# Performance work log

Measured on AMD Instinct MI355X. Metric: run time of the kernel, lower is better.

The kernel has to match this reference:

```python
import jax, jax.numpy as jnp
import numpy as np

N = 50000      # nodes
T = 24         # sequence length
D_IN = 16      # lstm input dim
H = 64         # lstm hidden dim
SD = 9         # static feature dim
G_IN, G_HID, G_OUT = 64, 64, 1
E = 1600000    # edges
NUM_GRAPHS = 500


def setup_inputs() -> dict:
    key = jax.random.key(0)
    ks = jax.random.split(key, 16)
    s = 0.1
    return {
        "x": jax.random.normal(ks[0], (N, T, D_IN), dtype=jnp.float32),
        "sdi": jax.random.normal(ks[1], (N, SD), dtype=jnp.float32),
        "edge_index": jax.random.randint(ks[2], (2, E), 0, N, dtype=jnp.int64),
        "batch": jnp.sort(jax.random.randint(ks[3], (N,), 0, NUM_GRAPHS, dtype=jnp.int64)),
        # LSTM params (torch gate order: i, f, g, o)
        "W_ih": s * jax.random.normal(ks[4], (4 * H, D_IN), dtype=jnp.float32),
        "W_hh": s * jax.random.normal(ks[5], (4 * H, H), dtype=jnp.float32),
        "b_ih": s * jax.random.normal(ks[6], (4 * H,), dtype=jnp.float32),
        "b_hh": s * jax.random.normal(ks[7], (4 * H,), dtype=jnp.float32),
        # Linear l1: (hidden + static) -> graph_input
        "l1_W": s * jax.random.normal(ks[8], (G_IN, H + SD), dtype=jnp.float32),
        "l1_b": s * jax.random.normal(ks[9], (G_IN,), dtype=jnp.float32),
        # GCNConv layers (weight stored [out, in] like torch Linear)
        "gcn1_W": s * jax.random.normal(ks[10], (G_HID, G_IN), dtype=jnp.float32),
        "gcn1_b": s * jax.random.normal(ks[11], (G_HID,), dtype=jnp.float32),
        "gcn2_W": s * jax.random.normal(ks[12], (G_OUT, G_HID), dtype=jnp.float32),
        "gcn2_b": s * jax.random.normal(ks[13], (G_OUT,), dtype=jnp.float32),
    }


def _lstm_last_hidden(x, W_ih, W_hh, b_ih, b_hh):
    # x: [N, T, D]; returns final hidden state h_T: [N, H]
    xg = jnp.einsum("ntd,gd->tng", x, W_ih) + (b_ih + b_hh)  # [T, N, 4H]
    h0 = jnp.zeros((x.shape[0], H), x.dtype)
    c0 = jnp.zeros((x.shape[0], H), x.dtype)

    def step(carry, g_t):
        h, c = carry
        g = g_t + h @ W_hh.T
        i, f, gg, o = jnp.split(g, 4, axis=-1)
        i = jax.nn.sigmoid(i)
        f = jax.nn.sigmoid(f)
        gg = jnp.tanh(gg)
        o = jax.nn.sigmoid(o)
        c = f * c + i * gg
        h = o * jnp.tanh(c)
        return (h, c), None

    (h, _), _ = jax.lax.scan(step, (h0, c0), xg)
    return h


def _gcn_conv(x, edge_index, W, b):
    # PyG GCNConv: add self-loops, symmetric normalization, scatter-add at dst.
    n = x.shape[0]
    loop = jnp.arange(n, dtype=edge_index.dtype)
    row = jnp.concatenate([edge_index[0], loop])  # src
    col = jnp.concatenate([edge_index[1], loop])  # dst
    deg = jax.ops.segment_sum(jnp.ones_like(col, dtype=x.dtype), col, num_segments=n)
    dis = jnp.where(deg > 0, jax.lax.rsqrt(jnp.maximum(deg, 1.0)), 0.0)
    norm = dis[row] * dis[col]                    # [E + N]
    h = x @ W.T                                   # [N, out]
    msg = h[row] * norm[:, None]                  # gather + scale
    out = jax.ops.segment_sum(msg, col, num_segments=n)
    return out + b


def reference(x, sdi, edge_index, batch, W_ih, W_hh, b_ih, b_hh,
              l1_W, l1_b, gcn1_W, gcn1_b, gcn2_W, gcn2_b):
    h = _lstm_last_hidden(x, W_ih, W_hh, b_ih, b_hh)       # [N, H]
    z = jnp.concatenate([h, sdi], axis=-1) @ l1_W.T + l1_b  # [N, G_IN]
    z = jax.nn.relu(_gcn_conv(z, edge_index, gcn1_W, gcn1_b))
    z = _gcn_conv(z, edge_index, gcn2_W, gcn2_b)            # [N, 1]
    # global mean pool over graph ids
    sums = jax.ops.segment_sum(z, batch, num_segments=NUM_GRAPHS)
    cnts = jax.ops.segment_sum(jnp.ones((z.shape[0],), z.dtype), batch, num_segments=NUM_GRAPHS)
    pooled = sums / jnp.maximum(cnts, 1.0)[:, None]         # [G, 1]
    return pooled.reshape(-1)
```

## Files before the change

### kernel.cpp

```cpp
#include <hip/hip_runtime.h>
#include <hip/hip_bf16.h>

#define N_NODES 50000
#define T_SEQ 24
#define D_IN 16
#define H_DIM 64
#define SD 9
#define E_EDGES 1600000
#define NUM_GRAPHS 500
#define NBLK 196

typedef _Float16 half8 __attribute__((ext_vector_type(8)));
typedef _Float16 half4 __attribute__((ext_vector_type(4)));
typedef float floatx4 __attribute__((ext_vector_type(4)));

__device__ __forceinline__ float fsig(float x) {
    return __fdividef(1.0f, 1.0f + __expf(-x));
}
__device__ __forceinline__ float ftanh(float x) {
    return 1.0f - __fdividef(2.0f, 1.0f + __expf(2.0f * x));
}

__global__ __launch_bounds__(256, 2) void lstm_mfma(
    const float* __restrict__ x,
    const float* __restrict__ W_ih, const float* __restrict__ W_hh,
    const float* __restrict__ b_ih, const float* __restrict__ b_hh,
    const float* __restrict__ Wc, const float* __restrict__ bc,
    const float* __restrict__ sdi, const float* __restrict__ dis,
    float* __restrict__ m_out)
{
    __shared__ _Float16 smem[2048 + 24 * 16 * 16];
    _Float16* hb0 = smem;
    _Float16* hb1 = smem + 1024;
    _Float16* xbuf = smem + 2048;

    const int tid  = threadIdx.x;
    const int lane = tid & 63;
    const int w    = tid >> 6;
    const int lr   = lane & 15;
    const int lg   = lane >> 4;
    const int nbase = blockIdx.x * 16;

    half8 bw[4][3];
    float bias[4];
#pragma unroll
    for (int ct = 0; ct < 4; ct++) {
        const int r = ct * 64 + w * 16 + lr;
        bias[ct] = b_ih[r] + b_hh[r];
#pragma unroll
        for (int kt = 0; kt < 2; kt++) {
            const float* p = W_hh + r * 64 + kt * 32 + 8 * lg;
            half8 f;
#pragma unroll
            for (int e = 0; e < 8; e++) f[e] = (_Float16)p[e];
            bw[ct][kt] = f;
        }
        half8 f = {(_Float16)0, (_Float16)0, (_Float16)0, (_Float16)0,
                   (_Float16)0, (_Float16)0, (_Float16)0, (_Float16)0};
        if (lg < 2) {
            const float* p = W_ih + r * 16 + 8 * lg;
#pragma unroll
            for (int e = 0; e < 8; e++) f[e] = (_Float16)p[e];
        }
        bw[ct][2] = f;
    }

    half8 bwc[3];
    {
        const int fr = w * 16 + lr;
#pragma unroll
        for (int kt = 0; kt < 2; kt++) {
            const float* p = Wc + fr * 73 + kt * 32 + 8 * lg;
            half8 f;
#pragma unroll
            for (int e = 0; e < 8; e++) f[e] = (_Float16)p[e];
            bwc[kt] = f;
        }
        half8 f = {(_Float16)0, (_Float16)0, (_Float16)0, (_Float16)0,
                   (_Float16)0, (_Float16)0, (_Float16)0, (_Float16)0};
#pragma unroll
        for (int e = 0; e < 8; e++) {
            const int k2 = 8 * lg + e;
            if (k2 < 9) f[e] = (_Float16)Wc[fr * 73 + 64 + k2];
            else if (k2 == 9) f[e] = (_Float16)bc[fr];
        }
        bwc[2] = f;
    }

#pragma unroll
    for (int it = 0; it < 6; it++) {
        const int f4 = tid + it * 256;
        const int fi = f4 * 4;
        const int n  = fi / 384;
        const int rem = fi - n * 384;
        const int t  = rem >> 4;
        const int d  = rem & 15;
        const float4 v = *reinterpret_cast<const float4*>(
            x + (size_t)(nbase + n) * 384 + rem);
        half4 hv = {(_Float16)v.x, (_Float16)v.y, (_Float16)v.z, (_Float16)v.w};
        *reinterpret_cast<half4*>(&xbuf[t * 256 + n * 16 + d]) = hv;
    }
    if (tid < 128) { ((int*)hb0)[tid] = 0; ((int*)hb0)[tid + 128] = 0; ((int*)hb0)[tid + 256] = 0; ((int*)hb0)[tid + 384] = 0; }

    const int u = w * 16 + lr;
    int ra[2];
#pragma unroll
    for (int kt = 0; kt < 2; kt++)
        ra[kt] = lr * 64 + 8 * ((4 * kt + lg) ^ (lr & 7));
    int woff[4];
#pragma unroll
    for (int j = 0; j < 4; j++) {
        const int nj = 4 * lg + j;
        woff[j] = nj * 64 + (u & 7) + 8 * ((u >> 3) ^ (nj & 7));
    }
    const int xro = lr * 16 + 8 * (lg & 1);

    float c_reg[4];
#pragma unroll
    for (int j = 0; j < 4; j++) c_reg[j] = 0.0f;

    __syncthreads();

    auto step = [&](int tl, _Float16* hR, _Float16* hW) {
        floatx4 acc[4];
#pragma unroll
        for (int ct = 0; ct < 4; ct++) {
            floatx4 a = {bias[ct], bias[ct], bias[ct], bias[ct]};
            acc[ct] = a;
        }
        const half8 ax = *reinterpret_cast<const half8*>(&xbuf[tl * 256 + xro]);
        const half8 ah0 = *reinterpret_cast<const half8*>(&hR[ra[0]]);
        const half8 ah1 = *reinterpret_cast<const half8*>(&hR[ra[1]]);
#pragma unroll
        for (int ct = 0; ct < 4; ct++)
            acc[ct] = __builtin_amdgcn_mfma_f32_16x16x32_f16(ah0, bw[ct][0], acc[ct], 0, 0, 0);
#pragma unroll
        for (int ct = 0; ct < 4; ct++)
            acc[ct] = __builtin_amdgcn_mfma_f32_16x16x32_f16(ah1, bw[ct][1], acc[ct], 0, 0, 0);
#pragma unroll
        for (int ct = 0; ct < 4; ct++)
            acc[ct] = __builtin_amdgcn_mfma_f32_16x16x32_f16(ax, bw[ct][2], acc[ct], 0, 0, 0);

#pragma unroll
        for (int j = 0; j < 4; j++) {
            const float ig = fsig(acc[0][j]);
            const float fg = fsig(acc[1][j]);
            const float gg = ftanh(acc[2][j]);
            const float og = fsig(acc[3][j]);
            const float cv = fg * c_reg[j] + ig * gg;
            c_reg[j] = cv;
            const float hv = og * ftanh(cv);
            hW[woff[j]] = (_Float16)hv;
        }
        __syncthreads();
    };

    for (int tb = 0; tb < 6; tb++) {
        const int t0 = tb * 4;
        step(t0 + 0, hb0, hb1);
        step(t0 + 1, hb1, hb0);
        step(t0 + 2, hb0, hb1);
        step(t0 + 3, hb1, hb0);
    }

    half8 axs = {(_Float16)0, (_Float16)0, (_Float16)0, (_Float16)0,
                 (_Float16)0, (_Float16)0, (_Float16)0, (_Float16)0};
#pragma unroll
    for (int e = 0; e < 8; e++) {
        const int k2 = 8 * lg + e;
        if (k2 < 9) axs[e] = (_Float16)sdi[(size_t)(nbase + lr) * SD + k2];
        else if (k2 == 9) axs[e] = (_Float16)1.0f;
    }
    const half8 fh0 = *reinterpret_cast<const half8*>(&hb0[ra[0]]);
    const half8 fh1 = *reinterpret_cast<const half8*>(&hb0[ra[1]]);
    floatx4 am = {0.0f, 0.0f, 0.0f, 0.0f};
    am = __builtin_amdgcn_mfma_f32_16x16x32_f16(fh0, bwc[0], am, 0, 0, 0);
    am = __builtin_amdgcn_mfma_f32_16x16x32_f16(fh1, bwc[1], am, 0, 0, 0);
    am = __builtin_amdgcn_mfma_f32_16x16x32_f16(axs, bwc[2], am, 0, 0, 0);
#pragma unroll
    for (int j = 0; j < 4; j++) {
        const int gn = nbase + 4 * lg + j;
        m_out[(size_t)gn * 64 + u] = am[j] * dis[gn];
    }
}

__global__ void count_deg(const int* __restrict__ ei, int* __restrict__ cnt) {
    int e = blockIdx.x * 256 + threadIdx.x;
    if (e < E_EDGES) {
        int c = ei[E_EDGES + e];
        if ((unsigned)c < N_NODES) atomicAdd(&cnt[c], 1);
    }
}

__global__ __launch_bounds__(256) void scanA(const int* __restrict__ cnt,
                                             int* __restrict__ ptr,
                                             float* __restrict__ dis,
                                             int* __restrict__ bsum)
{
    __shared__ int wsum[4];
    const int tid = threadIdx.x, lane = tid & 63, wv = tid >> 6;
    const int i = blockIdx.x * 256 + tid;
    const int orig = (i < N_NODES) ? cnt[i] : 0;
    int v = orig;
#pragma unroll
    for (int d = 1; d < 64; d <<= 1) {
        int nb = __shfl_up(v, d, 64);
        if (lane >= d) v += nb;
    }
    if (lane == 63) wsum[wv] = v;
    __syncthreads();
    int woff = 0;
#pragma unroll
    for (int k = 0; k < 3; k++) if (k < wv) woff += wsum[k];
    if (i < N_NODES) {
        ptr[i] = woff + v - orig;
        dis[i] = rsqrtf((float)(orig + 1));
    }
    if (tid == 255) bsum[blockIdx.x] = woff + v;
}

__global__ __launch_bounds__(256) void scanB(const int* __restrict__ bsum,
                                             int* __restrict__ boff,
                                             int* __restrict__ ptr)
{
    __shared__ int wsum[4];
    const int tid = threadIdx.x, lane = tid & 63, wv = tid >> 6;
    const int orig = (tid < NBLK) ? bsum[tid] : 0;
    int v = orig;
#pragma unroll
    for (int d = 1; d < 64; d <<= 1) {
        int nb = __shfl_up(v, d, 64);
        if (lane >= d) v += nb;
    }
    if (lane == 63) wsum[wv] = v;
    __syncthreads();
    int woff = 0;
#pragma unroll
    for (int k = 0; k < 3; k++) if (k < wv) woff += wsum[k];
    if (tid < NBLK) boff[tid] = woff + v - orig;
    if (tid == 255) ptr[N_NODES] = woff + v;
}

__global__ __launch_bounds__(256) void scanC(int* __restrict__ ptr,
                                             const int* __restrict__ boff,
                                             int* __restrict__ cursor)
{
    const int i = blockIdx.x * 256 + threadIdx.x;
    if (i < N_NODES) {
        const int p = ptr[i] + boff[blockIdx.x];
        ptr[i] = p;
        cursor[i] = p;
    }
}

__global__ void fill_csr(const int* __restrict__ ei, int* __restrict__ cursor,
                         int* __restrict__ csr)
{
    int e = blockIdx.x * 256 + threadIdx.x;
    if (e < E_EDGES) {
        int r = ei[e];
        int c = ei[E_EDGES + e];
        if ((unsigned)r < N_NODES && (unsigned)c < N_NODES) {
            int slot = atomicAdd(&cursor[c], 1);
            csr[slot] = r;
        }
    }
}

__global__ void combine_w(const float* __restrict__ g1W, const float* __restrict__ l1W,
                          const float* __restrict__ l1b,
                          float* __restrict__ Wc, float* __restrict__ bc)
{
    int idx = blockIdx.x * 256 + threadIdx.x;
    int o = idx / 74, j = idx - o * 74;
    if (o >= 64) return;
    float acc = 0.0f;
    if (j < 73) {
#pragma unroll 8
        for (int k = 0; k < 64; k++) acc += g1W[o * 64 + k] * l1W[k * 73 + j];
        Wc[o * 73 + j] = acc;
    } else {
#pragma unroll 8
        for (int k = 0; k < 64; k++) acc += g1W[o * 64 + k] * l1b[k];
        bc[o] = acc;
    }
}

__global__ __launch_bounds__(256) void gatherfin1s2(
    const int* __restrict__ ptr, const int* __restrict__ csr,
    const float* __restrict__ m, const float* __restrict__ dis,
    const float* __restrict__ b1, const float* __restrict__ W2,
    float* __restrict__ s2)
{
    const int wid = (blockIdx.x * 256 + threadIdx.x) >> 6;
    const int f = threadIdx.x & 63;
    if (wid >= N_NODES) return;
    const int b = ptr[wid];
    const int e = ptr[wid + 1];
    float a0 = 0.0f, a1 = 0.0f, a2 = 0.0f, a3 = 0.0f;
    int i = b;
    for (; i + 4 <= e; i += 4) {
        const int s0 = csr[i], s1 = csr[i + 1], sc2 = csr[i + 2], s3 = csr[i + 3];
        a0 += m[(size_t)s0 * 64 + f];
        a1 += m[(size_t)s1 * 64 + f];
        a2 += m[(size_t)sc2 * 64 + f];
        a3 += m[(size_t)s3 * 64 + f];
    }
    for (; i < e; i++) a0 += m[(size_t)csr[i] * 64 + f];
    const float self = m[(size_t)wid * 64 + f];
    const float dn = dis[wid];
    const float v = dn * (((a0 + a1) + (a2 + a3)) + self) + b1[f];
    const float z1 = v > 0.0f ? v : 0.0f;
    float p = z1 * W2[f];
#pragma unroll
    for (int off = 32; off >= 1; off >>= 1) p += __shfl_xor(p, off, 64);
    if (f == 0) s2[wid] = dn * p;
}

__global__ void gather2fin(const int* __restrict__ ptr, const int* __restrict__ csr,
                           const float* __restrict__ s2, const float* __restrict__ dis,
                           const float* __restrict__ b2, const int* __restrict__ batch,
                           float* __restrict__ gsum, float* __restrict__ gcnt)
{
    int n = blockIdx.x * 256 + threadIdx.x;
    if (n >= N_NODES) return;
    const int b = ptr[n];
    const int e = ptr[n + 1];
    float a0 = 0.0f, a1 = 0.0f, a2 = 0.0f, a3 = 0.0f;
    int i = b;
    for (; i + 4 <= e; i += 4) {
        a0 += s2[csr[i]];
        a1 += s2[csr[i + 1]];
        a2 += s2[csr[i + 2]];
        a3 += s2[csr[i + 3]];
    }
    for (; i < e; i++) a0 += s2[csr[i]];
    const float z2 = dis[n] * (((a0 + a1) + (a2 + a3)) + s2[n]) + b2[0];
    const int g = batch[n];
    if ((unsigned)g < NUM_GRAPHS) {
        atomicAdd(&gsum[g], z2);
        atomicAdd(&gcnt[g], 1.0f);
    }
}

__global__ void pooldiv(const float* __restrict__ gsum, const float* __restrict__ gcnt,
                        float* __restrict__ out)
{
    int g = blockIdx.x * 256 + threadIdx.x;
    if (g < NUM_GRAPHS) out[g] = gsum[g] / fmaxf(gcnt[g], 1.0f);
}

extern "C" void kernel_launch(void* const* d_in, const int* in_sizes, int n_in,
                              void* d_out, int out_size, void* d_ws, size_t ws_size,
                              hipStream_t stream)
{
    const float* x     = (const float*)d_in[0];
    const float* sdi   = (const float*)d_in[1];
    const int*   ei    = (const int*)d_in[2];
    const int*   batch = (const int*)d_in[3];
    const float* W_ih  = (const float*)d_in[4];
    const float* W_hh  = (const float*)d_in[5];
    const float* b_ih  = (const float*)d_in[6];
    const float* b_hh  = (const float*)d_in[7];
    const float* l1_W  = (const float*)d_in[8];
    const float* l1_b  = (const float*)d_in[9];
    const float* g1_W  = (const float*)d_in[10];
    const float* g1_b  = (const float*)d_in[11];
    const float* g2_W  = (const float*)d_in[12];
    const float* g2_b  = (const float*)d_in[13];
    float* out = (float*)d_out;

    float* ws   = (float*)d_ws;
    float* C    = ws + 6400000;
    float* dis  = ws + 9600000;
    float* s2   = dis + 50000;
    float* gsum = s2 + 50000;
    float* gcnt = gsum + 500;
    int* cnt    = (int*)(gcnt + 500);
    int* ptr    = cnt + 50000;
    int* cursor = ptr + 50001;
    int* csr    = cursor + 50000;
    float* Wc   = (float*)(csr + E_EDGES);
    float* bc   = Wc + 64 * 73;
    int* bsum   = (int*)(bc + 64);
    int* boff   = bsum + NBLK;

    const int featBlocks = (N_NODES * 64 + 255) / 256;
    const int edgeBlocks = (E_EDGES + 255) / 256;

    hipMemsetAsync(cnt, 0, 50000 * sizeof(int), stream);
    hipMemsetAsync(gsum, 0, 1000 * sizeof(float), stream);
    count_deg<<<edgeBlocks, 256, 0, stream>>>(ei, cnt);
    scanA<<<NBLK, 256, 0, stream>>>(cnt, ptr, dis, bsum);
    scanB<<<1, 256, 0, stream>>>(bsum, boff, ptr);
    scanC<<<NBLK, 256, 0, stream>>>(ptr, boff, cursor);
    fill_csr<<<edgeBlocks, 256, 0, stream>>>(ei, cursor, csr);
    combine_w<<<(64 * 74 + 255) / 256, 256, 0, stream>>>(g1_W, l1_W, l1_b, Wc, bc);

    lstm_mfma<<<N_NODES / 16, 256, 0, stream>>>(x, W_ih, W_hh, b_ih, b_hh,
                                                Wc, bc, sdi, dis, C);

    gatherfin1s2<<<featBlocks, 256, 0, stream>>>(ptr, csr, C, dis, g1_b, g2_W, s2);

    gather2fin<<<NBLK, 256, 0, stream>>>(ptr, csr, s2, dis, g2_b, batch, gsum, gcnt);
    pooldiv<<<2, 256, 0, stream>>>(gsum, gcnt, out);
}
```

Baseline: 551.9 us.

## Fuse degree counting into LSTM kernel and defer source normalization to gather

Moves the edge-degree atomic counting into the start of the LSTM kernel, which now runs before the scan, so the separate count_deg launch disappears and its memory traffic can overlap with LSTM compute. Because dis is not yet available when the LSTM runs, the source-side normalization moves into the first gather, which reads dis[src] per edge. The gsum/gcnt memset is folded into scanB. This saves kernel launches but adds a dis load per edge in the gather and puts atomics at the front of the LSTM kernel.

```diff
diff --git a/kernel.cpp b/kernel.cpp
--- a/kernel.cpp
+++ b/kernel.cpp
@@ -9,6 +9,7 @@
 #define E_EDGES 1600000
 #define NUM_GRAPHS 500
 #define NBLK 196
+#define LSTM_BLOCKS 3125
 
 typedef _Float16 half8 __attribute__((ext_vector_type(8)));
 typedef _Float16 half4 __attribute__((ext_vector_type(4)));
@@ -26,7 +27,8 @@
     const float* __restrict__ W_ih, const float* __restrict__ W_hh,
     const float* __restrict__ b_ih, const float* __restrict__ b_hh,
     const float* __restrict__ Wc, const float* __restrict__ bc,
-    const float* __restrict__ sdi, const float* __restrict__ dis,
+    const float* __restrict__ sdi,
+    const int* __restrict__ ei, int* __restrict__ cnt,
     float* __restrict__ m_out)
 {
     __shared__ _Float16 smem[2048 + 24 * 16 * 16];
@@ -40,6 +42,11 @@
     const int lr   = lane & 15;
     const int lg   = lane >> 4;
     const int nbase = blockIdx.x * 16;
+
+    for (int e = blockIdx.x * 256 + tid; e < E_EDGES; e += LSTM_BLOCKS * 256) {
+        const int c = ei[E_EDGES + e];
+        if ((unsigned)c < N_NODES) atomicAdd(&cnt[c], 1);
+    }
 
     half8 bw[4][3];
     float bias[4];
@@ -180,15 +187,7 @@
 #pragma unroll
     for (int j = 0; j < 4; j++) {
         const int gn = nbase + 4 * lg + j;
-        m_out[(size_t)gn * 64 + u] = am[j] * dis[gn];
-    }
-}
-
-__global__ void count_deg(const int* __restrict__ ei, int* __restrict__ cnt) {
-    int e = blockIdx.x * 256 + threadIdx.x;
-    if (e < E_EDGES) {
-        int c = ei[E_EDGES + e];
-        if ((unsigned)c < N_NODES) atomicAdd(&cnt[c], 1);
+        m_out[(size_t)gn * 64 + u] = am[j];
     }
 }
 
@@ -221,10 +220,13 @@
 
 __global__ __launch_bounds__(256) void scanB(const int* __restrict__ bsum,
                                              int* __restrict__ boff,
-                                             int* __restrict__ ptr)
+                                             int* __restrict__ ptr,
+                                             float* __restrict__ gzero)
 {
     __shared__ int wsum[4];
     const int tid = threadIdx.x, lane = tid & 63, wv = tid >> 6;
+#pragma unroll
+    for (int k = 0; k < 4; k++) gzero[tid + k * 256] = 0.0f;
     const int orig = (tid < NBLK) ? bsum[tid] : 0;
     int v = orig;
 #pragma unroll
@@ -301,14 +303,15 @@
     int i = b;
     for (; i + 4 <= e; i += 4) {
         const int s0 = csr[i], s1 = csr[i + 1], sc2 = csr[i + 2], s3 = csr[i + 3];
-        a0 += m[(size_t)s0 * 64 + f];
-        a1 += m[(size_t)s1 * 64 + f];
-        a2 += m[(size_t)sc2 * 64 + f];
-        a3 += m[(size_t)s3 * 64 + f];
-    }
-    for (; i < e; i++) a0 += m[(size_t)csr[i] * 64 + f];
-    const float self = m[(size_t)wid * 64 + f];
+        const float d0 = dis[s0], d1 = dis[s1], d2 = dis[sc2], d3 = dis[s3];
+        a0 += d0 * m[(size_t)s0 * 64 + f];
+        a1 += d1 * m[(size_t)s1 * 64 + f];
+        a2 += d2 * m[(size_t)sc2 * 64 + f];
+        a3 += d3 * m[(size_t)s3 * 64 + f];
+    }
+    for (; i < e; i++) { const int s = csr[i]; a0 += dis[s] * m[(size_t)s * 64 + f]; }
     const float dn = dis[wid];
+    const float self = dn * m[(size_t)wid * 64 + f];
     const float v = dn * (((a0 + a1) + (a2 + a3)) + self) + b1[f];
     const float z1 = v > 0.0f ? v : 0.0f;
     float p = z1 * W2[f];
@@ -376,7 +379,7 @@
     float* s2   = dis + 50000;
     float* gsum = s2 + 50000;
     float* gcnt = gsum + 500;
-    int* cnt    = (int*)(gcnt + 500);
+    int* cnt    = (int*)(gsum + 1024);
     int* ptr    = cnt + 50000;
     int* cursor = ptr + 50001;
     int* csr    = cursor + 50000;
@@ -389,16 +392,15 @@
     const int edgeBlocks = (E_EDGES + 255) / 256;
 
     hipMemsetAsync(cnt, 0, 50000 * sizeof(int), stream);
-    hipMemsetAsync(gsum, 0, 1000 * sizeof(float), stream);
-    count_deg<<<edgeBlocks, 256, 0, stream>>>(ei, cnt);
+    combine_w<<<(64 * 74 + 255) / 256, 256, 0, stream>>>(g1_W, l1_W, l1_b, Wc, bc);
+
+    lstm_mfma<<<LSTM_BLOCKS, 256, 0, stream>>>(x, W_ih, W_hh, b_ih, b_hh,
+                                               Wc, bc, sdi, ei, cnt, C);
+
     scanA<<<NBLK, 256, 0, stream>>>(cnt, ptr, dis, bsum);
-    scanB<<<1, 256, 0, stream>>>(bsum, boff, ptr);
+    scanB<<<1, 256, 0, stream>>>(bsum, boff, ptr, gsum);
     scanC<<<NBLK, 256, 0, stream>>>(ptr, boff, cursor);
     fill_csr<<<edgeBlocks, 256, 0, stream>>>(ei, cursor, csr);
-    combine_w<<<(64 * 74 + 255) / 256, 256, 0, stream>>>(g1_W, l1_W, l1_b, Wc, bc);
-
-    lstm_mfma<<<N_NODES / 16, 256, 0, stream>>>(x, W_ih, W_hh, b_ih, b_hh,
-                                                Wc, bc, sdi, dis, C);
 
     gatherfin1s2<<<featBlocks, 256, 0, stream>>>(ptr, csr, C, dis, g1_b, g2_W, s2);
 
```

Result: faster. 491.0 us (-11.0%).
